# Kernel tuning notes

Measured on AMD Instinct MI355X. Metric: run time of the kernel, lower is better.

The kernel has to match this reference:

```python
import jax, jax.numpy as jnp
import numpy as np

B, N = 4096, 1024


def setup_inputs() -> dict:
    key = jax.random.key(0)
    k1, k2 = jax.random.split(key)
    cors = 0.1 * jax.random.normal(k1, (B, N, 3), dtype=jnp.float32)  # predicted correspondences/offsets
    p_src = jax.random.normal(k2, (B, N, 3), dtype=jnp.float32)       # source point cloud
    return {"cors": cors, "p_src": p_src}


def reference(cors, p_src):
    # p_pred = p_src + cors  (target points implied by correspondences)
    p_pred = p_src + cors
    # centroids over the point dimension: [B, 1, 3]
    src_centroid = jnp.mean(p_src, axis=1, keepdims=True)
    pred_centroid = jnp.mean(p_pred, axis=1, keepdims=True)
    src_trans = p_src - src_centroid
    pred_trans = p_pred - pred_centroid
    # 3x3 cross-covariance per batch: h = src_trans^T @ pred_trans  -> [B, 3, 3]
    h = jnp.einsum('bnd,bne->bde', src_trans, pred_trans)
    # tf.linalg.svd returns s, u, v with h = u diag(s) v^T; jnp returns u, s, vh with vh = v^T
    u, s, vh = jnp.linalg.svd(h, full_matrices=False)
    # r_est = v @ u^T = (u @ vh)^T
    r_est = jnp.swapaxes(jnp.matmul(u, vh), -1, -2)  # [B, 3, 3]
    # t_est = -r_est @ src_centroid^T + pred_centroid^T  -> [B, 3, 1]
    t_est = -jnp.matmul(r_est, jnp.swapaxes(src_centroid, -1, -2)) + jnp.swapaxes(pred_centroid, -1, -2)
    g_top = jnp.concatenate([r_est, t_est], axis=2)  # [B, 3, 4]
    last_row = jnp.broadcast_to(
        jnp.array([[[0.0, 0.0, 0.0, 1.0]]], dtype=g_top.dtype), (g_top.shape[0], 1, 4)
    )
    return jnp.concatenate([g_top, last_row], axis=1)  # [B, 4, 4]
```

## Files before the change

kernel.cpp:

```cpp
#include <hip/hip_runtime.h>


constexpr int NPTS  = 1024;
constexpr int WAVES = 4;
constexpr int THREADS = WAVES * 64;

__global__ __launch_bounds__(THREADS) void svd_layer_kernel(
    const float* __restrict__ cors,
    const float* __restrict__ p_src,
    float* __restrict__ out,
    int B)
{
    const int wave = threadIdx.x >> 6;
    const int lane = threadIdx.x & 63;
    const int b    = blockIdx.x * WAVES + wave;
    if (b >= B) return;

    const size_t base4 = (size_t)b * (NPTS * 3 / 4);
    const float4* s4 = reinterpret_cast<const float4*>(p_src) + base4 + lane * 12;
    const float4* c4 = reinterpret_cast<const float4*>(cors)  + base4 + lane * 12;

    float4 sv[12], cv[12];
    #pragma unroll
    for (int m = 0; m < 12; ++m) sv[m] = s4[m];
    #pragma unroll
    for (int m = 0; m < 12; ++m) cv[m] = c4[m];

    float acc[15];
    #pragma unroll
    for (int i = 0; i < 15; ++i) acc[i] = 0.f;

    #pragma unroll
    for (int g = 0; g < 4; ++g) {
        const float4 t0 = sv[g*3+0], t1 = sv[g*3+1], t2 = sv[g*3+2];
        const float4 u0 = cv[g*3+0], u1 = cv[g*3+1], u2 = cv[g*3+2];
        const float sx[4] = {t0.x, t0.w, t1.z, t2.y};
        const float sy[4] = {t0.y, t1.x, t1.w, t2.z};
        const float sz[4] = {t0.z, t1.y, t2.x, t2.w};
        const float px[4] = {sx[0]+u0.x, sx[1]+u0.w, sx[2]+u1.z, sx[3]+u2.y};
        const float py[4] = {sy[0]+u0.y, sy[1]+u1.x, sy[2]+u1.w, sy[3]+u2.z};
        const float pz[4] = {sz[0]+u0.z, sz[1]+u1.y, sz[2]+u2.x, sz[3]+u2.w};
        #pragma unroll
        for (int k = 0; k < 4; ++k) {
            acc[0]  += sx[k]; acc[1]  += sy[k]; acc[2]  += sz[k];
            acc[3]  += px[k]; acc[4]  += py[k]; acc[5]  += pz[k];
            acc[6]  += sx[k]*px[k]; acc[7]  += sx[k]*py[k]; acc[8]  += sx[k]*pz[k];
            acc[9]  += sy[k]*px[k]; acc[10] += sy[k]*py[k]; acc[11] += sy[k]*pz[k];
            acc[12] += sz[k]*px[k]; acc[13] += sz[k]*py[k]; acc[14] += sz[k]*pz[k];
        }
    }

    #pragma unroll
    for (int off = 32; off > 0; off >>= 1) {
        #pragma unroll
        for (int i = 0; i < 15; ++i) acc[i] += __shfl_down(acc[i], off, 64);
    }

    if (lane != 0) return;

    const float invN = 1.0f / (float)NPTS;
    const float cs[3] = {acc[0]*invN, acc[1]*invN, acc[2]*invN};
    const float cp[3] = {acc[3]*invN, acc[4]*invN, acc[5]*invN};

    float Hm[3][3];
    #pragma unroll
    for (int i = 0; i < 3; ++i)
        #pragma unroll
        for (int j = 0; j < 3; ++j)
            Hm[i][j] = acc[6 + i*3 + j] - (float)NPTS * cs[i] * cp[j];

    float K[3][3];
    #pragma unroll
    for (int i = 0; i < 3; ++i)
        #pragma unroll
        for (int j = 0; j < 3; ++j)
            K[i][j] = Hm[0][i]*Hm[0][j] + Hm[1][i]*Hm[1][j] + Hm[2][i]*Hm[2][j];

    const float tr3 = (K[0][0] + K[1][1] + K[2][2]) * (1.0f/3.0f);
    const float is  = 1.0f / fmaxf(tr3, 1e-30f);

    float Y[3][3], Z[3][3];
    #pragma unroll
    for (int i = 0; i < 3; ++i)
        #pragma unroll
        for (int j = 0; j < 3; ++j) {
            Y[i][j] = K[i][j] * is;
            Z[i][j] = (i == j) ? 1.0f : 0.0f;
        }

    #pragma unroll
    for (int it = 0; it < 6; ++it) {
        float W[3][3];
        #pragma unroll
        for (int i = 0; i < 3; ++i)
            #pragma unroll
            for (int j = 0; j < 3; ++j) {
                float w = Z[i][0]*Y[0][j] + Z[i][1]*Y[1][j] + Z[i][2]*Y[2][j];
                W[i][j] = ((i == j) ? 1.5f : 0.0f) - 0.5f * w;
            }
        float Yn[3][3], Zn[3][3];
        #pragma unroll
        for (int i = 0; i < 3; ++i)
            #pragma unroll
            for (int j = 0; j < 3; ++j) {
                Yn[i][j] = Y[i][0]*W[0][j] + Y[i][1]*W[1][j] + Y[i][2]*W[2][j];
                Zn[i][j] = W[i][0]*Z[0][j] + W[i][1]*Z[1][j] + W[i][2]*Z[2][j];
            }
        #pragma unroll
        for (int i = 0; i < 3; ++i)
            #pragma unroll
            for (int j = 0; j < 3; ++j) { Y[i][j] = Yn[i][j]; Z[i][j] = Zn[i][j]; }
    }

    const float rs = rsqrtf(fmaxf(tr3, 1e-30f));
    float R[3][3];
    #pragma unroll
    for (int i = 0; i < 3; ++i)
        #pragma unroll
        for (int j = 0; j < 3; ++j)
            R[i][j] = (Z[i][0]*Hm[j][0] + Z[i][1]*Hm[j][1] + Z[i][2]*Hm[j][2]) * rs;

    const float t0 = cp[0] - (R[0][0]*cs[0] + R[0][1]*cs[1] + R[0][2]*cs[2]);
    const float t1 = cp[1] - (R[1][0]*cs[0] + R[1][1]*cs[1] + R[1][2]*cs[2]);
    const float t2 = cp[2] - (R[2][0]*cs[0] + R[2][1]*cs[1] + R[2][2]*cs[2]);

    float4* o4 = reinterpret_cast<float4*>(out + (size_t)b * 16);
    o4[0] = make_float4(R[0][0], R[0][1], R[0][2], t0);
    o4[1] = make_float4(R[1][0], R[1][1], R[1][2], t1);
    o4[2] = make_float4(R[2][0], R[2][1], R[2][2], t2);
    o4[3] = make_float4(0.f, 0.f, 0.f, 1.f);
}

extern "C" void kernel_launch(void* const* d_in, const int* in_sizes, int n_in,
                              void* d_out, int out_size, void* d_ws, size_t ws_size,
                              hipStream_t stream)
{
    const float* cors  = (const float*)d_in[0];
    const float* p_src = (const float*)d_in[1];
    float* out = (float*)d_out;
    const int B = in_sizes[0] / (NPTS * 3);
    const int grid = (B + WAVES - 1) / WAVES;
    hipLaunchKernelGGL(svd_layer_kernel, dim3(grid), dim3(THREADS), 0, stream,
                       cors, p_src, out, B);
}
```

Before: 134.0 us.

## Map one batch per block with coalesced loads staged through LDS

Each block now processes a single batch instead of one batch per wave. Threads issue fully coalesced float4 loads (stride-1 across the block), stage them in LDS, and then read back xyz-aligned triples. Partial sums are reduced within each wave by shuffles and across the four waves through shared memory. This targets the strided per-lane 12-float4 loads of the old layout, which coalesced poorly and held many registers. The cost is about 24KB of LDS per block, two barriers, and a serial SVD tail on one thread per block.

```diff
diff --git a/kernel.cpp b/kernel.cpp
--- a/kernel.cpp
+++ b/kernel.cpp
@@ -1,53 +1,52 @@
 #include <hip/hip_runtime.h>
 
 
-constexpr int NPTS  = 1024;
-constexpr int WAVES = 4;
-constexpr int THREADS = WAVES * 64;
+constexpr int NPTS    = 1024;
+constexpr int THREADS = 256;
+constexpr int NF4     = NPTS * 3 / 4;
 
 __global__ __launch_bounds__(THREADS) void svd_layer_kernel(
     const float* __restrict__ cors,
     const float* __restrict__ p_src,
-    float* __restrict__ out,
-    int B)
+    float* __restrict__ out)
 {
-    const int wave = threadIdx.x >> 6;
-    const int lane = threadIdx.x & 63;
-    const int b    = blockIdx.x * WAVES + wave;
-    if (b >= B) return;
+    __shared__ float4 lds_s[NF4];
+    __shared__ float4 lds_c[NF4];
+    __shared__ float  red[4][15];
 
-    const size_t base4 = (size_t)b * (NPTS * 3 / 4);
-    const float4* s4 = reinterpret_cast<const float4*>(p_src) + base4 + lane * 12;
-    const float4* c4 = reinterpret_cast<const float4*>(cors)  + base4 + lane * 12;
+    const int b = blockIdx.x;
+    const int t = threadIdx.x;
+    const int wave = t >> 6, lane = t & 63;
 
-    float4 sv[12], cv[12];
-    #pragma unroll
-    for (int m = 0; m < 12; ++m) sv[m] = s4[m];
-    #pragma unroll
-    for (int m = 0; m < 12; ++m) cv[m] = c4[m];
+    const float4* s4 = reinterpret_cast<const float4*>(p_src) + (size_t)b * NF4;
+    const float4* c4 = reinterpret_cast<const float4*>(cors)  + (size_t)b * NF4;
+
+    float4 a0 = s4[t], a1 = s4[t + 256], a2 = s4[t + 512];
+    float4 b0 = c4[t], b1 = c4[t + 256], b2 = c4[t + 512];
+    lds_s[t] = a0; lds_s[t + 256] = a1; lds_s[t + 512] = a2;
+    lds_c[t] = b0; lds_c[t + 256] = b1; lds_c[t + 512] = b2;
+    __syncthreads();
+
+    const float4 t0 = lds_s[t*3+0], t1 = lds_s[t*3+1], t2 = lds_s[t*3+2];
+    const float4 u0 = lds_c[t*3+0], u1 = lds_c[t*3+1], u2 = lds_c[t*3+2];
+
+    const float sx[4] = {t0.x, t0.w, t1.z, t2.y};
+    const float sy[4] = {t0.y, t1.x, t1.w, t2.z};
+    const float sz[4] = {t0.z, t1.y, t2.x, t2.w};
+    const float px[4] = {sx[0]+u0.x, sx[1]+u0.w, sx[2]+u1.z, sx[3]+u2.y};
+    const float py[4] = {sy[0]+u0.y, sy[1]+u1.x, sy[2]+u1.w, sy[3]+u2.z};
+    const float pz[4] = {sz[0]+u0.z, sz[1]+u1.y, sz[2]+u2.x, sz[3]+u2.w};
 
     float acc[15];
     #pragma unroll
     for (int i = 0; i < 15; ++i) acc[i] = 0.f;
-
     #pragma unroll
-    for (int g = 0; g < 4; ++g) {
-        const float4 t0 = sv[g*3+0], t1 = sv[g*3+1], t2 = sv[g*3+2];
-        const float4 u0 = cv[g*3+0], u1 = cv[g*3+1], u2 = cv[g*3+2];
-        const float sx[4] = {t0.x, t0.w, t1.z, t2.y};
-        const float sy[4] = {t0.y, t1.x, t1.w, t2.z};
-        const float sz[4] = {t0.z, t1.y, t2.x, t2.w};
-        const float px[4] = {sx[0]+u0.x, sx[1]+u0.w, sx[2]+u1.z, sx[3]+u2.y};
-        const float py[4] = {sy[0]+u0.y, sy[1]+u1.x, sy[2]+u1.w, sy[3]+u2.z};
-        const float pz[4] = {sz[0]+u0.z, sz[1]+u1.y, sz[2]+u2.x, sz[3]+u2.w};
-        #pragma unroll
-        for (int k = 0; k < 4; ++k) {
-            acc[0]  += sx[k]; acc[1]  += sy[k]; acc[2]  += sz[k];
-            acc[3]  += px[k]; acc[4]  += py[k]; acc[5]  += pz[k];
-            acc[6]  += sx[k]*px[k]; acc[7]  += sx[k]*py[k]; acc[8]  += sx[k]*pz[k];
-            acc[9]  += sy[k]*px[k]; acc[10] += sy[k]*py[k]; acc[11] += sy[k]*pz[k];
-            acc[12] += sz[k]*px[k]; acc[13] += sz[k]*py[k]; acc[14] += sz[k]*pz[k];
-        }
+    for (int k = 0; k < 4; ++k) {
+        acc[0]  += sx[k]; acc[1]  += sy[k]; acc[2]  += sz[k];
+        acc[3]  += px[k]; acc[4]  += py[k]; acc[5]  += pz[k];
+        acc[6]  += sx[k]*px[k]; acc[7]  += sx[k]*py[k]; acc[8]  += sx[k]*pz[k];
+        acc[9]  += sy[k]*px[k]; acc[10] += sy[k]*py[k]; acc[11] += sy[k]*pz[k];
+        acc[12] += sz[k]*px[k]; acc[13] += sz[k]*py[k]; acc[14] += sz[k]*pz[k];
     }
 
     #pragma unroll
@@ -56,18 +55,28 @@
         for (int i = 0; i < 15; ++i) acc[i] += __shfl_down(acc[i], off, 64);
     }
 
-    if (lane != 0) return;
+    if (lane == 0) {
+        #pragma unroll
+        for (int i = 0; i < 15; ++i) red[wave][i] = acc[i];
+    }
+    __syncthreads();
+    if (t != 0) return;
+
+    float S[15];
+    #pragma unroll
+    for (int i = 0; i < 15; ++i)
+        S[i] = red[0][i] + red[1][i] + red[2][i] + red[3][i];
 
     const float invN = 1.0f / (float)NPTS;
-    const float cs[3] = {acc[0]*invN, acc[1]*invN, acc[2]*invN};
-    const float cp[3] = {acc[3]*invN, acc[4]*invN, acc[5]*invN};
+    const float cs[3] = {S[0]*invN, S[1]*invN, S[2]*invN};
+    const float cp[3] = {S[3]*invN, S[4]*invN, S[5]*invN};
 
     float Hm[3][3];
     #pragma unroll
     for (int i = 0; i < 3; ++i)
         #pragma unroll
         for (int j = 0; j < 3; ++j)
-            Hm[i][j] = acc[6 + i*3 + j] - (float)NPTS * cs[i] * cp[j];
+            Hm[i][j] = S[6 + i*3 + j] - (float)NPTS * cs[i] * cp[j];
 
     float K[3][3];
     #pragma unroll
@@ -120,14 +129,14 @@
         for (int j = 0; j < 3; ++j)
             R[i][j] = (Z[i][0]*Hm[j][0] + Z[i][1]*Hm[j][1] + Z[i][2]*Hm[j][2]) * rs;
 
-    const float t0 = cp[0] - (R[0][0]*cs[0] + R[0][1]*cs[1] + R[0][2]*cs[2]);
-    const float t1 = cp[1] - (R[1][0]*cs[0] + R[1][1]*cs[1] + R[1][2]*cs[2]);
-    const float t2 = cp[2] - (R[2][0]*cs[0] + R[2][1]*cs[1] + R[2][2]*cs[2]);
+    const float tx = cp[0] - (R[0][0]*cs[0] + R[0][1]*cs[1] + R[0][2]*cs[2]);
+    const float ty = cp[1] - (R[1][0]*cs[0] + R[1][1]*cs[1] + R[1][2]*cs[2]);
+    const float tz = cp[2] - (R[2][0]*cs[0] + R[2][1]*cs[1] + R[2][2]*cs[2]);
 
     float4* o4 = reinterpret_cast<float4*>(out + (size_t)b * 16);
-    o4[0] = make_float4(R[0][0], R[0][1], R[0][2], t0);
-    o4[1] = make_float4(R[1][0], R[1][1], R[1][2], t1);
-    o4[2] = make_float4(R[2][0], R[2][1], R[2][2], t2);
+    o4[0] = make_float4(R[0][0], R[0][1], R[0][2], tx);
+    o4[1] = make_float4(R[1][0], R[1][1], R[1][2], ty);
+    o4[2] = make_float4(R[2][0], R[2][1], R[2][2], tz);
     o4[3] = make_float4(0.f, 0.f, 0.f, 1.f);
 }
 
@@ -139,7 +148,6 @@
     const float* p_src = (const float*)d_in[1];
     float* out = (float*)d_out;
     const int B = in_sizes[0] / (NPTS * 3);
-    const int grid = (B + WAVES - 1) / WAVES;
-    hipLaunchKernelGGL(svd_layer_kernel, dim3(grid), dim3(THREADS), 0, stream,
-                       cors, p_src, out, B);
+    hipLaunchKernelGGL(svd_layer_kernel, dim3(B), dim3(THREADS), 0, stream,
+                       cors, p_src, out);
 }
```

Result: faster. 118.7 us (-11.4%).
